# Kernel optimization log

Measured on AMD Instinct MI355X. Metric: run time of the kernel, lower is better.

Reference implementation:

```python
import jax, jax.numpy as jnp
import numpy as np

B, T, H = 64, 1024, 1024


def setup_inputs() -> dict:
    key = jax.random.key(0)
    ks = jax.random.split(key, 8)
    s = 1.0 / np.sqrt(H)
    return {
        "spatial_feats": jax.random.normal(ks[0], (B, T, H), dtype=jnp.float32),
        "hidden_state": jax.random.normal(ks[1], (B, H), dtype=jnp.float32),
        "W_enc": jax.random.uniform(ks[2], (H, H), jnp.float32, -s, s),
        "b_enc": jax.random.uniform(ks[3], (H,), jnp.float32, -s, s),
        "W_dec": jax.random.uniform(ks[4], (H, H), jnp.float32, -s, s),
        "b_dec": jax.random.uniform(ks[5], (H,), jnp.float32, -s, s),
        "w_score": jax.random.uniform(ks[6], (H,), jnp.float32, -s, s),
        "b_score": jax.random.uniform(ks[7], (), jnp.float32, -s, s),
    }


def reference(spatial_feats, hidden_state, W_enc, b_enc, W_dec, b_dec, w_score, b_score):
    # decoder_proj(hidden_state): [B, H] -> [B, 1, H]
    dec = (jnp.einsum("bh,oh->bo", hidden_state, W_dec) + b_dec)[:, None, :]
    # encoder_proj(spatial_feats): [B, T, H]
    enc = jnp.einsum("bth,oh->bto", spatial_feats, W_enc) + b_enc
    energy = jnp.tanh(enc + dec)                      # [B, T, H]
    scores = jnp.einsum("bth,h->bt", energy, w_score) + b_score  # [B, T]
    weights = jax.nn.softmax(scores, axis=1)          # [B, T]
    context = jnp.einsum("bth,bt->bh", spatial_feats, weights)   # [B, H]
    return (context, weights)
```

## Files before the change

### kernel.cpp

```cpp
#include <hip/hip_runtime.h>
#include <hip/hip_bf16.h>
#include <math.h>


typedef __attribute__((ext_vector_type(8))) short bf16x8;
typedef __attribute__((ext_vector_type(8))) unsigned short ushort8;
typedef __attribute__((ext_vector_type(4))) float f32x4;

__device__ __forceinline__ unsigned short f2bf(float f) {
  union { float f; unsigned int u; } v; v.f = f;
  unsigned int r = v.u + 0x7FFFu + ((v.u >> 16) & 1u);
  return (unsigned short)(r >> 16);
}

__device__ __forceinline__ float bf2f(unsigned short b) {
  union { unsigned int u; float f; } v; v.u = ((unsigned int)b) << 16;
  return v.f;
}

__device__ __forceinline__ float fast_tanh(float x) {
  float e = __expf(2.0f * x);
  return 1.0f - 2.0f / (e + 1.0f);
}

__device__ __forceinline__ void gld16(const void* g, void* l) {
  __builtin_amdgcn_global_load_lds(
      (const __attribute__((address_space(1))) void*)g,
      (__attribute__((address_space(3))) void*)l, 16, 0, 0);
}

__global__ __launch_bounds__(256) void prep_kernel(
    const float* __restrict__ spatial, const float* __restrict__ hidden,
    const float* __restrict__ W_enc, const float* __restrict__ b_enc,
    const float* __restrict__ W_dec, const float* __restrict__ b_dec,
    unsigned short* __restrict__ Wbf, unsigned short* __restrict__ Abf,
    float* __restrict__ dec, int nCvt) {
  __shared__ float hs[1024];
  const int bid = blockIdx.x, tid = threadIdx.x;
  if (bid < nCvt) {
    const bool isW = bid < 32;
    const float* src = isW ? W_enc : spatial;
    unsigned short* dst = isW ? Wbf : Abf;
    const size_t base = (size_t)(isW ? bid : bid - 32) * 8192 + tid;
    #pragma unroll 4
    for (int i = 0; i < 32; i++) {
      size_t g4 = base + (size_t)i * 256;
      float4 v = ((const float4*)src)[g4];
      ushort4 o;
      o.x = f2bf(v.x); o.y = f2bf(v.y); o.z = f2bf(v.z); o.w = f2bf(v.w);
      *(ushort4*)(dst + g4 * 4) = o;
    }
    return;
  }
  const int dbid = bid - nCvt;
  const int b = dbid >> 3, o0 = (dbid & 7) * 128;
  const int wave = tid >> 6, lane = tid & 63;
  ((float4*)hs)[tid] = ((const float4*)(hidden + (size_t)b * 1024))[tid];
  __syncthreads();
  for (int it = 0; it < 32; it++) {
    int o = o0 + it * 4 + wave;
    const float4* w4 = (const float4*)(W_dec + (size_t)o * 1024);
    float4 acc; acc.x = acc.y = acc.z = acc.w = 0.f;
    #pragma unroll
    for (int j = 0; j < 4; j++) {
      int i = j * 64 + lane;
      float4 x = ((const float4*)hs)[i], y = w4[i];
      acc.x = fmaf(x.x, y.x, acc.x);
      acc.y = fmaf(x.y, y.y, acc.y);
      acc.z = fmaf(x.z, y.z, acc.z);
      acc.w = fmaf(x.w, y.w, acc.w);
    }
    float v = (acc.x + acc.y) + (acc.z + acc.w);
    #pragma unroll
    for (int off = 1; off < 64; off <<= 1) v += __shfl_xor(v, off);
    if (lane == 0) dec[b * 1024 + o] = v + b_dec[o] + b_enc[o];
  }
}

__global__ __launch_bounds__(512, 2) void enc_score_bf16_kernel(
    const unsigned short* __restrict__ A,
    const unsigned short* __restrict__ W,
    const float* __restrict__ dec,
    const float* __restrict__ w_score,
    float* __restrict__ scores_p)
{
  __shared__ unsigned short As[2][256][64];
  __shared__ unsigned short Bs[2][256][64];

  const int bid = blockIdx.x;
  const int swz = (bid & 7) * 128 + (bid >> 3);
  const int nt = swz & 3;
  const int m0 = (swz >> 2) * 256;
  const int n0 = nt * 256;
  const int tid = threadIdx.x;
  const int lane = tid & 63, wave = tid >> 6;
  const int wm = (wave >> 2) * 128;
  const int wn = (wave & 3) * 64;
  const int quad = lane >> 4, colL = lane & 15;

  const int s_rowoff = wave * 16 + (lane >> 3);
  const int s_col = ((lane & 7) ^ (lane >> 3)) * 8;
  const unsigned short* gA = A + (size_t)m0 * 1024;
  const unsigned short* gB = W + (size_t)n0 * 1024;

  auto stageA = [&](int kt, int h) {
    const unsigned short* src =
        gA + (size_t)(h * 128 + s_rowoff) * 1024 + kt * 64 + s_col;
    unsigned short* dst = &As[kt & 1][h * 128 + wave * 16][0];
    gld16(src, dst);
    gld16(src + 8 * 1024, dst + 8 * 64);
  };
  auto stageB = [&](int kt, int h) {
    const unsigned short* src =
        gB + (size_t)(h * 128 + s_rowoff) * 1024 + kt * 64 + s_col;
    unsigned short* dst = &Bs[kt & 1][h * 128 + wave * 16][0];
    gld16(src, dst);
    gld16(src + 8 * 1024, dst + 8 * 64);
  };

  const int xs0 = ((0 * 4 + quad) ^ (colL & 7)) * 8;
  const int xs1 = ((1 * 4 + quad) ^ (colL & 7)) * 8;

  f32x4 acc[8][4];
  #pragma unroll
  for (int mi = 0; mi < 8; mi++)
    #pragma unroll
    for (int ni = 0; ni < 4; ni++)
      acc[mi][ni] = (f32x4){0.f, 0.f, 0.f, 0.f};

  stageA(0, 0); stageA(0, 1); stageB(0, 0); stageB(0, 1);
  stageB(1, 0); stageB(1, 1);
  asm volatile("s_waitcnt vmcnt(4)" ::: "memory");
  __builtin_amdgcn_s_barrier();

  auto ktile = [&](int kt, int buf) {
    bf16x8 bfr[4][2];
    #pragma unroll
    for (int q = 0; q < 4; q++) {
      bf16x8 af[2][2];
      #pragma unroll
      for (int mj = 0; mj < 2; mj++) {
        const int row = wm + (q * 2 + mj) * 16 + colL;
        af[mj][0] = *(const bf16x8*)&As[buf][row][xs0];
        af[mj][1] = *(const bf16x8*)&As[buf][row][xs1];
      }
      if (q == 0) {
        #pragma unroll
        for (int ni = 0; ni < 4; ni++) {
          const int row = wn + ni * 16 + colL;
          bfr[ni][0] = *(const bf16x8*)&Bs[buf][row][xs0];
          bfr[ni][1] = *(const bf16x8*)&Bs[buf][row][xs1];
        }
      }
      if (q == 0 && kt + 1 < 16) stageA(kt + 1, 0);
      if (q == 1 && kt + 1 < 16) stageA(kt + 1, 1);
      if (q == 2 && kt + 2 < 16) stageB(kt + 2, 0);
      if (q == 3 && kt + 2 < 16) stageB(kt + 2, 1);
      __builtin_amdgcn_s_barrier();
      asm volatile("s_waitcnt lgkmcnt(0)" ::: "memory");
      __builtin_amdgcn_s_setprio(1);
      #pragma unroll
      for (int s = 0; s < 2; s++)
        #pragma unroll
        for (int mj = 0; mj < 2; mj++)
          #pragma unroll
          for (int ni = 0; ni < 4; ni++)
            acc[q * 2 + mj][ni] = __builtin_amdgcn_mfma_f32_16x16x32_bf16(
                af[mj][s], bfr[ni][s], acc[q * 2 + mj][ni], 0, 0, 0);
      __builtin_amdgcn_s_setprio(0);
      if (q == 3) {
        if (kt + 2 < 16) asm volatile("s_waitcnt vmcnt(4)" ::: "memory");
        else             asm volatile("s_waitcnt vmcnt(0)" ::: "memory");
      }
      __builtin_amdgcn_s_barrier();
    }
  };

  for (int ku = 0; ku < 16; ku += 2) {
    ktile(ku, 0);
    ktile(ku + 1, 1);
  }

  const int b = m0 >> 10;
  float decv[4], wsv[4];
  #pragma unroll
  for (int ni = 0; ni < 4; ni++) {
    int n = n0 + wn + ni * 16 + colL;
    decv[ni] = dec[b * 1024 + n];
    wsv[ni] = w_score[n];
  }
  const int slot = nt * 4 + (wave & 3);
  #pragma unroll
  for (int mi = 0; mi < 8; mi++) {
    float rs[4] = {0.f, 0.f, 0.f, 0.f};
    #pragma unroll
    for (int ni = 0; ni < 4; ni++)
      #pragma unroll
      for (int r = 0; r < 4; r++)
        rs[r] += fast_tanh(acc[mi][ni][r] + decv[ni]) * wsv[ni];
    #pragma unroll
    for (int r = 0; r < 4; r++) {
      float v = rs[r];
      v += __shfl_xor(v, 1);
      v += __shfl_xor(v, 2);
      v += __shfl_xor(v, 4);
      v += __shfl_xor(v, 8);
      if (colL == 0)
        scores_p[slot * 65536 + m0 + wm + mi * 16 + quad * 4 + r] = v;
    }
  }
}

__global__ __launch_bounds__(256) void enc_score_f32_kernel(
    const float* __restrict__ A, const float* __restrict__ W,
    const float* __restrict__ dec, const float* __restrict__ w_score,
    float* __restrict__ scores_p) {
  __shared__ unsigned short As[128][32];
  __shared__ unsigned short Bs[128][32];
  const int bid = blockIdx.x;
  const int n0 = (bid & 7) * 128;
  const int m0 = (bid >> 3) * 128;
  const int tid = threadIdx.x;
  const int lane = tid & 63, wave = tid >> 6;
  const int wm = (wave >> 1) * 64, wn = (wave & 1) * 64;
  const int quad = lane >> 4, colL = lane & 15;
  const int srow = tid >> 3;
  const int scol = (tid & 7) * 4;
  f32x4 acc[4][4];
  #pragma unroll
  for (int mi = 0; mi < 4; mi++)
    #pragma unroll
    for (int ni = 0; ni < 4; ni++)
      acc[mi][ni] = (f32x4){0.f, 0.f, 0.f, 0.f};
  for (int k0 = 0; k0 < 1024; k0 += 32) {
    #pragma unroll
    for (int p = 0; p < 4; p++) {
      int r = p * 32 + srow;
      float4 va = *(const float4*)(A + (size_t)(m0 + r) * 1024 + (k0 + scol));
      float4 vb = *(const float4*)(W + (size_t)(n0 + r) * 1024 + (k0 + scol));
      ushort4 pa, pb;
      pa.x = f2bf(va.x); pa.y = f2bf(va.y); pa.z = f2bf(va.z); pa.w = f2bf(va.w);
      pb.x = f2bf(vb.x); pb.y = f2bf(vb.y); pb.z = f2bf(vb.z); pb.w = f2bf(vb.w);
      *(ushort4*)(&As[r][scol]) = pa;
      *(ushort4*)(&Bs[r][scol]) = pb;
    }
    __syncthreads();
    bf16x8 af[4], bfr[4];
    #pragma unroll
    for (int i = 0; i < 4; i++) {
      af[i]  = *(const bf16x8*)(&As[wm + i * 16 + colL][quad * 8]);
      bfr[i] = *(const bf16x8*)(&Bs[wn + i * 16 + colL][quad * 8]);
    }
    #pragma unroll
    for (int mi = 0; mi < 4; mi++)
      #pragma unroll
      for (int ni = 0; ni < 4; ni++)
        acc[mi][ni] = __builtin_amdgcn_mfma_f32_16x16x32_bf16(
            af[mi], bfr[ni], acc[mi][ni], 0, 0, 0);
    __syncthreads();
  }
  const int b = m0 >> 10;
  float decv[4], wsv[4];
  #pragma unroll
  for (int ni = 0; ni < 4; ni++) {
    int n = n0 + wn + ni * 16 + colL;
    decv[ni] = dec[b * 1024 + n];
    wsv[ni] = w_score[n];
  }
  const int slot = (bid & 7) * 2 + (wave & 1);
  #pragma unroll
  for (int mi = 0; mi < 4; mi++) {
    float rsv[4] = {0.f, 0.f, 0.f, 0.f};
    #pragma unroll
    for (int ni = 0; ni < 4; ni++)
      #pragma unroll
      for (int r = 0; r < 4; r++)
        rsv[r] += fast_tanh(acc[mi][ni][r] + decv[ni]) * wsv[ni];
    #pragma unroll
    for (int r = 0; r < 4; r++) {
      float v = rsv[r];
      v += __shfl_xor(v, 1);
      v += __shfl_xor(v, 2);
      v += __shfl_xor(v, 4);
      v += __shfl_xor(v, 8);
      if (colL == 0)
        scores_p[slot * 65536 + m0 + wm + mi * 16 + quad * 4 + r] = v;
    }
  }
}

__global__ void softmax_kernel(const float* __restrict__ scores_p,
                               float* __restrict__ weights,
                               float* __restrict__ context) {
  __shared__ float red[256];
  int b = blockIdx.x, tid = threadIdx.x;
  float4 z; z.x = z.y = z.z = z.w = 0.f;
  ((float4*)context)[blockIdx.x * 256 + tid] = z;
  float v[4];
  float mx = -1e30f;
  #pragma unroll
  for (int i = 0; i < 4; i++) {
    int m = b * 1024 + tid + i * 256;
    float s = 0.f;
    #pragma unroll
    for (int sl = 0; sl < 16; sl++) s += scores_p[sl * 65536 + m];
    v[i] = s;
    mx = fmaxf(mx, v[i]);
  }
  red[tid] = mx; __syncthreads();
  for (int off = 128; off > 0; off >>= 1) {
    if (tid < off) red[tid] = fmaxf(red[tid], red[tid + off]);
    __syncthreads();
  }
  mx = red[0]; __syncthreads();
  float sum = 0.f;
  #pragma unroll
  for (int i = 0; i < 4; i++) { v[i] = __expf(v[i] - mx); sum += v[i]; }
  red[tid] = sum; __syncthreads();
  for (int off = 128; off > 0; off >>= 1) {
    if (tid < off) red[tid] += red[tid + off];
    __syncthreads();
  }
  float inv = 1.0f / red[0];
  #pragma unroll
  for (int i = 0; i < 4; i++) weights[b * 1024 + tid + i * 256] = v[i] * inv;
}

__global__ void context_bf16_kernel(const unsigned short* __restrict__ Abf,
                                    const float* __restrict__ weights,
                                    float* __restrict__ context) {
  int b = blockIdx.x >> 3, tq = blockIdx.x & 7;
  int tid = threadIdx.x;
  __shared__ float wl[128];
  __shared__ float cs[128 * 8];
  if (tid < 128) wl[tid] = weights[b * 1024 + tq * 128 + tid];
  __syncthreads();
  const int hl = tid & 127, p = tid >> 7;
  const int h0 = hl * 8;
  const unsigned short* sp =
      Abf + ((size_t)(b * 1024 + tq * 128 + p)) * 1024 + h0;
  float acc[8];
  #pragma unroll
  for (int j = 0; j < 8; j++) acc[j] = 0.f;
  for (int t = 0; t < 128; t += 2) {
    float w = wl[t + p];
    ushort8 x = *(const ushort8*)(sp + (size_t)t * 1024);
    #pragma unroll
    for (int j = 0; j < 8; j++) acc[j] = fmaf(w, bf2f(x[j]), acc[j]);
  }
  if (p == 0) {
    #pragma unroll
    for (int j = 0; j < 8; j++) cs[hl * 8 + j] = acc[j];
  }
  __syncthreads();
  if (p == 1) {
    #pragma unroll
    for (int j = 0; j < 8; j++) cs[hl * 8 + j] += acc[j];
  }
  __syncthreads();
  if (p == 0) {
    #pragma unroll
    for (int j = 0; j < 8; j++)
      atomicAdd(&context[b * 1024 + h0 + j], cs[hl * 8 + j]);
  }
}

__global__ void context_f32_kernel(const float* __restrict__ spatial,
                                   const float* __restrict__ weights,
                                   float* __restrict__ context) {
  int b = blockIdx.x >> 3, tq = blockIdx.x & 7;
  int tid = threadIdx.x;
  __shared__ float wl[128];
  if (tid < 128) wl[tid] = weights[b * 1024 + tq * 128 + tid];
  __syncthreads();
  const float4* sp =
      (const float4*)(spatial + ((size_t)(b * 1024 + tq * 128)) * 1024);
  float4 acc; acc.x = acc.y = acc.z = acc.w = 0.f;
  #pragma unroll 4
  for (int t = 0; t < 128; t++) {
    float w = wl[t];
    float4 x = sp[(size_t)t * 256 + tid];
    acc.x = fmaf(w, x.x, acc.x);
    acc.y = fmaf(w, x.y, acc.y);
    acc.z = fmaf(w, x.z, acc.z);
    acc.w = fmaf(w, x.w, acc.w);
  }
  float* c = context + b * 1024 + tid * 4;
  atomicAdd(c + 0, acc.x);
  atomicAdd(c + 1, acc.y);
  atomicAdd(c + 2, acc.z);
  atomicAdd(c + 3, acc.w);
}

extern "C" void kernel_launch(void* const* d_in, const int* in_sizes, int n_in,
                              void* d_out, int out_size, void* d_ws, size_t ws_size,
                              hipStream_t stream) {
  const float* spatial  = (const float*)d_in[0];
  const float* hidden   = (const float*)d_in[1];
  const float* W_enc    = (const float*)d_in[2];
  const float* b_enc    = (const float*)d_in[3];
  const float* W_dec    = (const float*)d_in[4];
  const float* b_dec    = (const float*)d_in[5];
  const float* w_score  = (const float*)d_in[6];

  float* out      = (float*)d_out;
  float* context  = out;
  float* weights  = out + 65536;

  float* scores_p = (float*)d_ws;
  float* dec      = scores_p + 16 * 65536;
  unsigned short* Wbf = (unsigned short*)(dec + 65536);
  unsigned short* Abf = Wbf + 1024 * 1024;

  const size_t need =
      16ull * 65536 * 4 + 65536 * 4 + 2ull * 1024 * 1024 + 2ull * 65536 * 1024;

  if (ws_size >= need) {
    const int nCvt = 32 + 2048;
    prep_kernel<<<nCvt + 512, 256, 0, stream>>>(
        spatial, hidden, W_enc, b_enc, W_dec, b_dec, Wbf, Abf, dec, nCvt);
    enc_score_bf16_kernel<<<1024, 512, 0, stream>>>(Abf, Wbf, dec, w_score,
                                                    scores_p);
    softmax_kernel<<<64, 256, 0, stream>>>(scores_p, weights, context);
    context_bf16_kernel<<<512, 256, 0, stream>>>(Abf, weights, context);
  } else {
    prep_kernel<<<512, 256, 0, stream>>>(
        spatial, hidden, W_enc, b_enc, W_dec, b_dec, nullptr, nullptr, dec,
        0);
    enc_score_f32_kernel<<<4096, 256, 0, stream>>>(spatial, W_enc, dec,
                                                   w_score, scores_p);
    softmax_kernel<<<64, 256, 0, stream>>>(scores_p, weights, context);
    context_f32_kernel<<<512, 256, 0, stream>>>(spatial, weights, context);
  }
}
```

Measured before the change: 615.5 us.

## Fuse fp32-to-bf16 conversion of spatial feats into GEMM tile staging

Drops the separate pass that converted the 256 MB fp32 spatial tensor to a bf16 copy. The GEMM now loads fp32 A tiles into registers, converts them to bf16 and writes them to LDS. W tiles are also staged through registers instead of direct global-to-LDS loads. The context reduction reads the original fp32 tensor. This removes a full write and re-read of a 128 MB intermediate, but the GEMM now reads twice the A bytes, spends VALU on conversion and loses the async direct-to-LDS pipelining.

```diff
diff --git a/kernel.cpp b/kernel.cpp
--- a/kernel.cpp
+++ b/kernel.cpp
@@ -6,6 +6,7 @@
 typedef __attribute__((ext_vector_type(8))) short bf16x8;
 typedef __attribute__((ext_vector_type(8))) unsigned short ushort8;
 typedef __attribute__((ext_vector_type(4))) float f32x4;
+typedef __attribute__((ext_vector_type(4))) unsigned int u32x4;
 
 __device__ __forceinline__ unsigned short f2bf(float f) {
   union { float f; unsigned int u; } v; v.f = f;
@@ -13,20 +14,13 @@
   return (unsigned short)(r >> 16);
 }
 
-__device__ __forceinline__ float bf2f(unsigned short b) {
-  union { unsigned int u; float f; } v; v.u = ((unsigned int)b) << 16;
-  return v.f;
+__device__ __forceinline__ unsigned int pk2bf(float lo, float hi) {
+  return (unsigned int)f2bf(lo) | ((unsigned int)f2bf(hi) << 16);
 }
 
 __device__ __forceinline__ float fast_tanh(float x) {
   float e = __expf(2.0f * x);
   return 1.0f - 2.0f / (e + 1.0f);
-}
-
-__device__ __forceinline__ void gld16(const void* g, void* l) {
-  __builtin_amdgcn_global_load_lds(
-      (const __attribute__((address_space(1))) void*)g,
-      (__attribute__((address_space(3))) void*)l, 16, 0, 0);
 }
 
 __global__ __launch_bounds__(256) void prep_kernel(
@@ -38,10 +32,9 @@
   __shared__ float hs[1024];
   const int bid = blockIdx.x, tid = threadIdx.x;
   if (bid < nCvt) {
-    const bool isW = bid < 32;
-    const float* src = isW ? W_enc : spatial;
-    unsigned short* dst = isW ? Wbf : Abf;
-    const size_t base = (size_t)(isW ? bid : bid - 32) * 8192 + tid;
+    const float* src = W_enc;
+    unsigned short* dst = Wbf;
+    const size_t base = (size_t)bid * 8192 + tid;
     #pragma unroll 4
     for (int i = 0; i < 32; i++) {
       size_t g4 = base + (size_t)i * 256;
@@ -78,7 +71,7 @@
 }
 
 __global__ __launch_bounds__(512, 2) void enc_score_bf16_kernel(
-    const unsigned short* __restrict__ A,
+    const float* __restrict__ A,
     const unsigned short* __restrict__ W,
     const float* __restrict__ dec,
     const float* __restrict__ w_score,
@@ -98,29 +91,45 @@
   const int wn = (wave & 3) * 64;
   const int quad = lane >> 4, colL = lane & 15;
 
-  const int s_rowoff = wave * 16 + (lane >> 3);
-  const int s_col = ((lane & 7) ^ (lane >> 3)) * 8;
-  const unsigned short* gA = A + (size_t)m0 * 1024;
+  const int s_row = wave * 16 + (lane >> 3);
+  const int a_col = (lane & 7) * 8;
+  const int w_slot = ((lane & 7) ^ (lane >> 3)) * 8;
+  const float* gA = A + (size_t)m0 * 1024;
   const unsigned short* gB = W + (size_t)n0 * 1024;
-
-  auto stageA = [&](int kt, int h) {
-    const unsigned short* src =
-        gA + (size_t)(h * 128 + s_rowoff) * 1024 + kt * 64 + s_col;
-    unsigned short* dst = &As[kt & 1][h * 128 + wave * 16][0];
-    gld16(src, dst);
-    gld16(src + 8 * 1024, dst + 8 * 64);
-  };
-  auto stageB = [&](int kt, int h) {
-    const unsigned short* src =
-        gB + (size_t)(h * 128 + s_rowoff) * 1024 + kt * 64 + s_col;
-    unsigned short* dst = &Bs[kt & 1][h * 128 + wave * 16][0];
-    gld16(src, dst);
-    gld16(src + 8 * 1024, dst + 8 * 64);
-  };
 
   const int xs0 = ((0 * 4 + quad) ^ (colL & 7)) * 8;
   const int xs1 = ((1 * 4 + quad) ^ (colL & 7)) * 8;
 
+  float4 rA0[4], rA1[4];
+  u32x4  rB0[2], rB1[2];
+
+  auto issueA = [&](int kt, int h, float4* r) {
+    const float* src = gA + (size_t)(h * 128 + s_row) * 1024 + kt * 64 + a_col;
+    r[0] = *(const float4*)(src);
+    r[1] = *(const float4*)(src + 4);
+    r[2] = *(const float4*)(src + 8 * 1024);
+    r[3] = *(const float4*)(src + 8 * 1024 + 4);
+  };
+  auto issueB = [&](int kt, int h, u32x4* r) {
+    const unsigned short* src =
+        gB + (size_t)(h * 128 + s_row) * 1024 + kt * 64 + a_col;
+    r[0] = *(const u32x4*)(src);
+    r[1] = *(const u32x4*)(src + 8 * 1024);
+  };
+  auto writeA = [&](int buf, int h, const float4* r) {
+    u32x4 p0, p1;
+    p0[0] = pk2bf(r[0].x, r[0].y); p0[1] = pk2bf(r[0].z, r[0].w);
+    p0[2] = pk2bf(r[1].x, r[1].y); p0[3] = pk2bf(r[1].z, r[1].w);
+    p1[0] = pk2bf(r[2].x, r[2].y); p1[1] = pk2bf(r[2].z, r[2].w);
+    p1[2] = pk2bf(r[3].x, r[3].y); p1[3] = pk2bf(r[3].z, r[3].w);
+    *(u32x4*)(&As[buf][h * 128 + s_row][w_slot]) = p0;
+    *(u32x4*)(&As[buf][h * 128 + s_row + 8][w_slot]) = p1;
+  };
+  auto writeB = [&](int buf, int h, const u32x4* r) {
+    *(u32x4*)(&Bs[buf][h * 128 + s_row][w_slot]) = r[0];
+    *(u32x4*)(&Bs[buf][h * 128 + s_row + 8][w_slot]) = r[1];
+  };
+
   f32x4 acc[8][4];
   #pragma unroll
   for (int mi = 0; mi < 8; mi++)
@@ -128,9 +137,11 @@
     for (int ni = 0; ni < 4; ni++)
       acc[mi][ni] = (f32x4){0.f, 0.f, 0.f, 0.f};
 
-  stageA(0, 0); stageA(0, 1); stageB(0, 0); stageB(0, 1);
-  stageB(1, 0); stageB(1, 1);
-  asm volatile("s_waitcnt vmcnt(4)" ::: "memory");
+  issueA(0, 0, rA0); issueB(0, 0, rB0);
+  issueA(0, 1, rA1); issueB(0, 1, rB1);
+  writeA(0, 0, rA0); writeB(0, 0, rB0);
+  writeA(0, 1, rA1); writeB(0, 1, rB1);
+  asm volatile("s_waitcnt lgkmcnt(0)" ::: "memory");
   __builtin_amdgcn_s_barrier();
 
   auto ktile = [&](int kt, int buf) {
@@ -152,12 +163,16 @@
           bfr[ni][1] = *(const bf16x8*)&Bs[buf][row][xs1];
         }
       }
-      if (q == 0 && kt + 1 < 16) stageA(kt + 1, 0);
-      if (q == 1 && kt + 1 < 16) stageA(kt + 1, 1);
-      if (q == 2 && kt + 2 < 16) stageB(kt + 2, 0);
-      if (q == 3 && kt + 2 < 16) stageB(kt + 2, 1);
+      if (kt < 15) {
+        if (q == 0) { issueA(kt + 1, 0, rA0); issueB(kt + 1, 0, rB0); }
+        if (q == 1) { issueA(kt + 1, 1, rA1); issueB(kt + 1, 1, rB1); }
+        if (q == 2) { writeA(buf ^ 1, 0, rA0); writeB(buf ^ 1, 0, rB0); }
+        if (q == 3) { writeA(buf ^ 1, 1, rA1); writeB(buf ^ 1, 1, rB1); }
+      }
+      __builtin_amdgcn_sched_barrier(0);
       __builtin_amdgcn_s_barrier();
       asm volatile("s_waitcnt lgkmcnt(0)" ::: "memory");
+      __builtin_amdgcn_sched_barrier(0);
       __builtin_amdgcn_s_setprio(1);
       #pragma unroll
       for (int s = 0; s < 2; s++)
@@ -168,10 +183,6 @@
             acc[q * 2 + mj][ni] = __builtin_amdgcn_mfma_f32_16x16x32_bf16(
                 af[mj][s], bfr[ni][s], acc[q * 2 + mj][ni], 0, 0, 0);
       __builtin_amdgcn_s_setprio(0);
-      if (q == 3) {
-        if (kt + 2 < 16) asm volatile("s_waitcnt vmcnt(4)" ::: "memory");
-        else             asm volatile("s_waitcnt vmcnt(0)" ::: "memory");
-      }
       __builtin_amdgcn_s_barrier();
     }
   };
@@ -324,45 +335,6 @@
   float inv = 1.0f / red[0];
   #pragma unroll
   for (int i = 0; i < 4; i++) weights[b * 1024 + tid + i * 256] = v[i] * inv;
-}
-
-__global__ void context_bf16_kernel(const unsigned short* __restrict__ Abf,
-                                    const float* __restrict__ weights,
-                                    float* __restrict__ context) {
-  int b = blockIdx.x >> 3, tq = blockIdx.x & 7;
-  int tid = threadIdx.x;
-  __shared__ float wl[128];
-  __shared__ float cs[128 * 8];
-  if (tid < 128) wl[tid] = weights[b * 1024 + tq * 128 + tid];
-  __syncthreads();
-  const int hl = tid & 127, p = tid >> 7;
-  const int h0 = hl * 8;
-  const unsigned short* sp =
-      Abf + ((size_t)(b * 1024 + tq * 128 + p)) * 1024 + h0;
-  float acc[8];
-  #pragma unroll
-  for (int j = 0; j < 8; j++) acc[j] = 0.f;
-  for (int t = 0; t < 128; t += 2) {
-    float w = wl[t + p];
-    ushort8 x = *(const ushort8*)(sp + (size_t)t * 1024);
-    #pragma unroll
-    for (int j = 0; j < 8; j++) acc[j] = fmaf(w, bf2f(x[j]), acc[j]);
-  }
-  if (p == 0) {
-    #pragma unroll
-    for (int j = 0; j < 8; j++) cs[hl * 8 + j] = acc[j];
-  }
-  __syncthreads();
-  if (p == 1) {
-    #pragma unroll
-    for (int j = 0; j < 8; j++) cs[hl * 8 + j] += acc[j];
-  }
-  __syncthreads();
-  if (p == 0) {
-    #pragma unroll
-    for (int j = 0; j < 8; j++)
-      atomicAdd(&context[b * 1024 + h0 + j], cs[hl * 8 + j]);
-  }
 }
 
 __global__ void context_f32_kernel(const float* __restrict__ spatial,
@@ -410,19 +382,17 @@
   float* scores_p = (float*)d_ws;
   float* dec      = scores_p + 16 * 65536;
   unsigned short* Wbf = (unsigned short*)(dec + 65536);
-  unsigned short* Abf = Wbf + 1024 * 1024;
-
-  const size_t need =
-      16ull * 65536 * 4 + 65536 * 4 + 2ull * 1024 * 1024 + 2ull * 65536 * 1024;
+
+  const size_t need = 16ull * 65536 * 4 + 65536 * 4 + 2ull * 1024 * 1024;
 
   if (ws_size >= need) {
-    const int nCvt = 32 + 2048;
+    const int nCvt = 32;
     prep_kernel<<<nCvt + 512, 256, 0, stream>>>(
-        spatial, hidden, W_enc, b_enc, W_dec, b_dec, Wbf, Abf, dec, nCvt);
-    enc_score_bf16_kernel<<<1024, 512, 0, stream>>>(Abf, Wbf, dec, w_score,
-                                                    scores_p);
+        spatial, hidden, W_enc, b_enc, W_dec, b_dec, Wbf, nullptr, dec, nCvt);
+    enc_score_bf16_kernel<<<1024, 512, 0, stream>>>(spatial, Wbf, dec,
+                                                    w_score, scores_p);
     softmax_kernel<<<64, 256, 0, stream>>>(scores_p, weights, context);
-    context_bf16_kernel<<<512, 256, 0, stream>>>(Abf, weights, context);
+    context_f32_kernel<<<512, 256, 0, stream>>>(spatial, weights, context);
   } else {
     prep_kernel<<<512, 256, 0, stream>>>(
         spatial, hidden, W_enc, b_enc, W_dec, b_dec, nullptr, nullptr, dec,
```

After: 644.6 us. 1.05x slower.
